# Kernel tuning notes

Hardware: AMD Instinct MI355X
Metric: run time of the kernel (lower is better)

Reference implementation:

```python
import jax, jax.numpy as jnp
import numpy as np
from jax import lax

B_, L_, D_ = 4, 2048, 256
DI, NS, DC, DTR = 512, 16, 4, 16  # d_inner=2*D, d_state, d_conv, dt_rank=ceil(D/16)
DFF = 4 * D_


def setup_inputs():
    key = jax.random.key(0)
    ks = jax.random.split(key, 20)
    rn = lambda k, s, sc=0.02: jax.random.normal(k, s, jnp.float32) * sc
    return {
        "x": jax.random.normal(ks[0], (B_, L_, D_), jnp.float32),
        "in_proj_w": rn(ks[1], (2 * DI, D_)), "in_proj_b": jnp.zeros((2 * DI,), jnp.float32),
        "conv_w": rn(ks[2], (DI, DC), 0.1), "conv_b": jnp.zeros((DI,), jnp.float32),
        "x_proj_w": rn(ks[3], (DTR + 2 * NS, DI)),
        "dt_proj_w": rn(ks[4], (DI, DTR), 0.1), "dt_proj_b": rn(ks[5], (DI,), 0.5),
        "A_log": jnp.log(jnp.tile(jnp.arange(1, NS + 1, dtype=jnp.float32), (DI, 1))),
        "D_ssm": jnp.ones((DI,), jnp.float32),
        "out_proj_w": rn(ks[6], (D_, DI)), "out_proj_b": jnp.zeros((D_,), jnp.float32),
        "ln1_g": jnp.ones((D_,), jnp.float32), "ln1_b": jnp.zeros((D_,), jnp.float32),
        "fc1_w": rn(ks[7], (DFF, D_)), "fc1_b": jnp.zeros((DFF,), jnp.float32),
        "fc2_w": rn(ks[8], (D_, DFF)), "fc2_b": jnp.zeros((D_,), jnp.float32),
        "ln2_g": jnp.ones((D_,), jnp.float32), "ln2_b": jnp.zeros((D_,), jnp.float32),
    }


def _layer_norm(x, g, b, eps=1e-5):
    m = jnp.mean(x, -1, keepdims=True)
    v = jnp.mean((x - m) ** 2, -1, keepdims=True)
    return (x - m) / jnp.sqrt(v + eps) * g + b


def _mamba(x, in_proj_w, in_proj_b, conv_w, conv_b, x_proj_w, dt_proj_w, dt_proj_b, A_log, D_ssm, out_proj_w, out_proj_b):
    B, L, D = x.shape
    xz = x @ in_proj_w.T + in_proj_b                       # [B,L,2*DI]
    xi, z = jnp.split(xz, 2, axis=-1)
    # causal depthwise conv over time
    xc = jnp.transpose(xi, (0, 2, 1))                       # [B,DI,L]
    xc = lax.conv_general_dilated(xc, conv_w[:, None, :], (1,), [(DC - 1, 0)],
                                  dimension_numbers=("NCH", "OIH", "NCH"),
                                  feature_group_count=DI)
    xi = jax.nn.silu(jnp.transpose(xc + conv_b[None, :, None], (0, 2, 1)))  # [B,L,DI]
    x_dbl = xi @ x_proj_w.T                                 # [B,L,DTR+2*NS]
    dt, Bs, Cs = jnp.split(x_dbl, [DTR, DTR + NS], axis=-1)
    dt = jax.nn.softplus(dt @ dt_proj_w.T + dt_proj_b)      # [B,L,DI]
    A = -jnp.exp(A_log)                                     # [DI,NS]
    dA = jnp.exp(dt[..., None] * A)                         # [B,L,DI,NS]
    dBu = dt[..., None] * Bs[:, :, None, :] * xi[..., None]  # [B,L,DI,NS]
    dA_t = jnp.moveaxis(dA, 1, 0)
    dBu_t = jnp.moveaxis(dBu, 1, 0)
    C_t = jnp.moveaxis(Cs, 1, 0)                            # [L,B,NS]

    def step(h, inp):
        a, bu, c = inp
        h = a * h + bu                                      # [B,DI,NS]
        y = jnp.einsum("bdn,bn->bd", h, c)
        return h, y

    h0 = jnp.zeros((B, DI, NS), x.dtype)
    _, ys = lax.scan(step, h0, (dA_t, dBu_t, C_t))
    y = jnp.moveaxis(ys, 0, 1) + xi * D_ssm                 # [B,L,DI]
    y = y * jax.nn.silu(z)
    return y @ out_proj_w.T + out_proj_b


def reference(x, in_proj_w, in_proj_b, conv_w, conv_b, x_proj_w, dt_proj_w, dt_proj_b,
              A_log, D_ssm, out_proj_w, out_proj_b, ln1_g, ln1_b, fc1_w, fc1_b,
              fc2_w, fc2_b, ln2_g, ln2_b):
    gelu = lambda t: jax.nn.gelu(t, approximate=False)
    ssm = _mamba(x, in_proj_w, in_proj_b, conv_w, conv_b, x_proj_w, dt_proj_w,
                 dt_proj_b, A_log, D_ssm, out_proj_w, out_proj_b)
    y = _layer_norm(x + ssm, ln1_g, ln1_b)                  # dropout = identity (eval)
    ffn = gelu(gelu(y @ fc1_w.T + fc1_b) @ fc2_w.T + fc2_b)
    return _layer_norm(y + ffn, ln2_g, ln2_b)
```

## Files before the change

### kernel.cpp

```cpp
#include <hip/hip_runtime.h>

typedef __bf16 bf16x8 __attribute__((ext_vector_type(8)));
typedef float  f32x4  __attribute__((ext_vector_type(4)));

#define AS1 __attribute__((address_space(1)))
#define AS3 __attribute__((address_space(3)))

__device__ __forceinline__ float bf2f(ushort u) {
    union { unsigned int i; float f; } v; v.i = ((unsigned int)u) << 16; return v.f;
}
__device__ __forceinline__ ushort f2bf(float f) {
    union { float f; unsigned int i; } v; v.f = f;
    unsigned int i = v.i;
    unsigned int r = i + 0x7FFFu + ((i >> 16) & 1u);
    return (ushort)(r >> 16);
}
__device__ __forceinline__ float bflo(unsigned int u) { return bf2f((ushort)(u & 0xFFFFu)); }
__device__ __forceinline__ float bfhi(unsigned int u) { return bf2f((ushort)(u >> 16)); }
__device__ __forceinline__ float gelu_f(float v) {
    return 0.5f * v * (1.f + erff(v * 0.70710678118654752f));
}

__device__ __forceinline__ bool sniff_inline(const ushort* __restrict__ x) {
    const int lane = threadIdx.x & 63;
    int cnt = 0;
    #pragma unroll
    for (int r = 0; r < 4; r++) {
        const ushort u = x[lane + r * 64];
        const int e = (u >> 7) & 0xFF;
        if ((u & 0x7FFF) == 0 || (e >= 112 && e <= 141)) cnt++;
    }
    #pragma unroll
    for (int o = 32; o > 0; o >>= 1) cnt += __shfl_xor(cnt, o);
    return cnt >= 224;
}

struct CanonArgs {
    const void* src[20];
    int off[20];
    int total;
};

__launch_bounds__(256)
__global__ void canon_k(CanonArgs a, ushort* __restrict__ dst, ushort* __restrict__ xpw_pad,
                        const ushort* __restrict__ sniffx)
{
    const int i = blockIdx.x * 256 + threadIdx.x;
    if (i >= a.total) {
        const int j = i - a.total;
        if (j < 8192) xpw_pad[24576 + j] = 0;
        return;
    }
    const bool fl = sniff_inline(sniffx);
    int s = 0;
    #pragma unroll
    for (int t = 1; t < 20; t++) if (i >= a.off[t]) s = t;
    const int li = i - a.off[s];
    ushort v;
    if (fl) v = ((const ushort*)a.src[s])[li];
    else    v = f2bf(((const float*)a.src[s])[li]);
    dst[i] = v;
    if (s == 5) xpw_pad[li] = v;
}

template<int BM, int BN>
__launch_bounds__(256, 2)
__global__ void gemm_bt(const ushort* __restrict__ A, const ushort* __restrict__ W,
                        const ushort* __restrict__ bias, ushort* __restrict__ Cb,
                        int N, int K)
{
    constexpr int WMT = BM / 32;
    constexpr int WNT = BN / 32;
    __shared__ __align__(16) ushort As[BM * 32];
    __shared__ __align__(16) ushort Bs[BN * 32];
    const int tid  = threadIdx.x;
    const int wave = tid >> 6;
    const int lane = tid & 63;
    const int m0 = blockIdx.x * BM;
    const int n0 = blockIdx.y * BN;
    const int wm = (wave >> 1) * (BM / 2);
    const int wn = (wave & 1) * (BN / 2);
    const int lrow = lane & 15;
    const int quad = lane >> 4;

    f32x4 acc[WMT][WNT];
    #pragma unroll
    for (int i = 0; i < WMT; i++)
        #pragma unroll
        for (int j = 0; j < WNT; j++)
            #pragma unroll
            for (int r = 0; r < 4; r++) acc[i][j][r] = 0.f;

    for (int k0 = 0; k0 < K; k0 += 32) {
        #pragma unroll
        for (int t = 0; t < BM / 64; t++) {
            const int inst = t * 4 + wave;
            const int row  = inst * 16 + (lane >> 2);
            const int sub  = lane & 3;
            const ushort* gp = A + (size_t)(m0 + row) * K + (k0 + sub * 8);
            __builtin_amdgcn_global_load_lds((AS1 void*)(void*)gp,
                                             (AS3 void*)(As + inst * 512), 16, 0, 0);
        }
        #pragma unroll
        for (int t = 0; t < BN / 64; t++) {
            const int inst = t * 4 + wave;
            const int row  = inst * 16 + (lane >> 2);
            const int sub  = lane & 3;
            const ushort* gp = W + (size_t)(n0 + row) * K + (k0 + sub * 8);
            __builtin_amdgcn_global_load_lds((AS1 void*)(void*)gp,
                                             (AS3 void*)(Bs + inst * 512), 16, 0, 0);
        }
        __syncthreads();
        bf16x8 afr[WMT], bfr[WNT];
        #pragma unroll
        for (int i = 0; i < WMT; i++)
            afr[i] = *(const bf16x8*)&As[(wm + i * 16 + lrow) * 32 + quad * 8];
        #pragma unroll
        for (int j = 0; j < WNT; j++)
            bfr[j] = *(const bf16x8*)&Bs[(wn + j * 16 + lrow) * 32 + quad * 8];
        #pragma unroll
        for (int i = 0; i < WMT; i++)
            #pragma unroll
            for (int j = 0; j < WNT; j++)
                acc[i][j] = __builtin_amdgcn_mfma_f32_16x16x32_bf16(afr[i], bfr[j], acc[i][j], 0, 0, 0);
        __syncthreads();
    }

    #pragma unroll
    for (int i = 0; i < WMT; i++) {
        const int gm = m0 + wm + i * 16 + quad * 4;
        #pragma unroll
        for (int j = 0; j < WNT; j++) {
            const int gn = n0 + wn + j * 16 + lrow;
            const float bv = bf2f(bias[gn]);
            #pragma unroll
            for (int r = 0; r < 4; r++)
                Cb[(size_t)(gm + r) * N + gn] = f2bf(acc[i][j][r] + bv);
        }
    }
}

__launch_bounds__(512)
__global__ void convscan1_k(const ushort* __restrict__ xz, const ushort* __restrict__ cw,
                            const ushort* __restrict__ cb, const ushort* __restrict__ xpw_pad,
                            const ushort* __restrict__ dtw, const ushort* __restrict__ dtb,
                            const ushort* __restrict__ Alog,
                            float* __restrict__ xdbl, float* __restrict__ summ)
{
    __shared__ __align__(16) ushort xcs[32 * 520];
    __shared__ float XD[32 * 48];
    const int tid  = threadIdx.x;
    const int wave = tid >> 6;
    const int lane = tid & 63;
    const int lrow = lane & 15;
    const int quad = lane >> 4;
    const int c = blockIdx.x, b = blockIdx.y;
    const int t0 = b * 2048 + c * 32;

    {
        const int d8 = (tid & 63) * 8;
        ushort wl[32];
        *(uint4*)&wl[0]  = *(const uint4*)&cw[d8 * 4];
        *(uint4*)&wl[8]  = *(const uint4*)&cw[d8 * 4 + 8];
        *(uint4*)&wl[16] = *(const uint4*)&cw[d8 * 4 + 16];
        *(uint4*)&wl[24] = *(const uint4*)&cw[d8 * 4 + 24];
        ushort bl[8];
        *(uint4*)&bl[0] = *(const uint4*)&cb[d8];
        #pragma unroll
        for (int it = 0; it < 4; it++) {
            const int trow = it * 8 + (tid >> 6);
            const int t = t0 + trow;
            const int l = t & 2047;
            float acc[8];
            #pragma unroll
            for (int j = 0; j < 8; j++) acc[j] = bf2f(bl[j]);
            #pragma unroll
            for (int k = 0; k < 4; k++) {
                const int ls = l - 3 + k;
                if (ls >= 0) {
                    ushort xl[8];
                    *(uint4*)&xl[0] = *(const uint4*)&xz[(size_t)(t - 3 + k) * 1024 + d8];
                    #pragma unroll
                    for (int j = 0; j < 8; j++) acc[j] += bf2f(xl[j]) * bf2f(wl[j * 4 + k]);
                }
            }
            ushort ol[8];
            #pragma unroll
            for (int j = 0; j < 8; j++) {
                const float s = acc[j] / (1.f + __expf(-acc[j]));
                ol[j] = f2bf(s);
            }
            *(uint4*)&xcs[trow * 520 + d8] = *(uint4*)&ol[0];
        }
    }
    __syncthreads();

    {
        const int mt = wave >> 2, nt = wave & 3;
        const ushort* bptr = xpw_pad + (size_t)(nt * 16 + lrow) * 512 + quad * 8;
        f32x4 acc = {0.f, 0.f, 0.f, 0.f};
        bf16x8 bn = *(const bf16x8*)bptr;
        for (int k0 = 0; k0 < 512; k0 += 32) {
            const bf16x8 bc = bn;
            if (k0 + 32 < 512) bn = *(const bf16x8*)(bptr + k0 + 32);
            const bf16x8 afr = *(const bf16x8*)&xcs[(mt * 16 + lrow) * 520 + k0 + quad * 8];
            acc = __builtin_amdgcn_mfma_f32_16x16x32_bf16(afr, bc, acc, 0, 0, 0);
        }
        const int col = nt * 16 + lrow;
        if (col < 48) {
            #pragma unroll
            for (int r = 0; r < 4; r++) {
                const int row = mt * 16 + quad * 4 + r;
                XD[row * 48 + col] = acc[r];
                xdbl[(size_t)(t0 + row) * 64 + col] = acc[r];
            }
        }
    }
    __syncthreads();

    {
        const int d = tid;
        const uint4 w0 = *(const uint4*)&dtw[d * 16];
        const uint4 w1 = *(const uint4*)&dtw[d * 16 + 8];
        const float wd[16] = { bflo(w0.x), bfhi(w0.x), bflo(w0.y), bfhi(w0.y),
                               bflo(w0.z), bfhi(w0.z), bflo(w0.w), bfhi(w0.w),
                               bflo(w1.x), bfhi(w1.x), bflo(w1.y), bfhi(w1.y),
                               bflo(w1.z), bfhi(w1.z), bflo(w1.w), bfhi(w1.w) };
        const float dtbv = bf2f(dtb[d]);
        float A[16], h[16];
        #pragma unroll
        for (int n = 0; n < 16; n++) {
            A[n] = -__expf(bf2f(Alog[d * 16 + n]));
            h[n] = 0.f;
        }
        float sdt = 0.f;
        for (int i = 0; i < 32; i++) {
            const float* Xr = &XD[i * 48];
            float s = dtbv;
            #pragma unroll
            for (int k = 0; k < 16; k++) s += Xr[k] * wd[k];
            const float dtv = (s > 15.f) ? s : __logf(1.f + __expf(s));
            const float xiv = bf2f(xcs[i * 520 + d]);
            const float dx = dtv * xiv;
            sdt += dtv;
            #pragma unroll
            for (int n = 0; n < 16; n++) {
                const float da = __expf(dtv * A[n]);
                h[n] = da * h[n] + dx * Xr[16 + n];
            }
        }
        const size_t base = ((size_t)(b * 64 + c) * 32) * 512 + d;
        #pragma unroll
        for (int n = 0; n < 16; n++) summ[base + (size_t)n * 512] = __expf(A[n] * sdt);
        #pragma unroll
        for (int n = 0; n < 16; n++) summ[base + (size_t)(16 + n) * 512] = h[n];
    }
}

__launch_bounds__(512)
__global__ void combine_k(float* __restrict__ summ)
{
    const int b = blockIdx.x >> 4, n = blockIdx.x & 15;
    const int d = threadIdx.x;
    float h = 0.f;
    #pragma unroll
    for (int half = 0; half < 2; half++) {
        float p[32], hl[32], ho[32];
        #pragma unroll
        for (int c2 = 0; c2 < 32; c2++) {
            const size_t sb = ((size_t)((b * 64 + half * 32 + c2) * 32 + n)) * 512 + d;
            p[c2]  = summ[sb];
            hl[c2] = summ[sb + 8192];
        }
        #pragma unroll
        for (int c2 = 0; c2 < 32; c2++) {
            ho[c2] = h;
            h = p[c2] * h + hl[c2];
        }
        #pragma unroll
        for (int c2 = 0; c2 < 32; c2++) {
            const size_t sb = ((size_t)((b * 64 + half * 32 + c2) * 32 + n)) * 512 + d;
            summ[sb] = ho[c2];
        }
    }
}

__launch_bounds__(512)
__global__ void tail_k(const ushort* __restrict__ xz, const ushort* __restrict__ cw,
                       const ushort* __restrict__ cb, const float* __restrict__ xdbl,
                       const ushort* __restrict__ dtw, const ushort* __restrict__ dtb,
                       const ushort* __restrict__ Alog, const float* __restrict__ summ,
                       const ushort* __restrict__ Dssm, const ushort* __restrict__ cx,
                       const ushort* __restrict__ opw, const ushort* __restrict__ opb,
                       const ushort* __restrict__ ln1g, const ushort* __restrict__ ln1b,
                       const ushort* __restrict__ f1w, const ushort* __restrict__ f1b,
                       const ushort* __restrict__ f2w, const ushort* __restrict__ f2b,
                       const ushort* __restrict__ ln2g, const ushort* __restrict__ ln2b,
                       void* __restrict__ dout, const ushort* __restrict__ sniffx)
{
    __shared__ __align__(16) ushort yls[32 * 520];
    __shared__ float XD[32 * 48];
    __shared__ __align__(16) ushort y1bs[32 * 264];
    __shared__ float redS[8 * 32], redQ[8 * 32];
    ushort* f1q = yls;

    const int tid  = threadIdx.x;
    const int wave = tid >> 6;
    const int lane = tid & 63;
    const int lrow = lane & 15;
    const int quad = lane >> 4;
    const int c = blockIdx.x, b = blockIdx.y;
    const int t0 = b * 2048 + c * 32;
    const int n0w = wave * 32;

    {
        const int d8 = (tid & 63) * 8;
        ushort wl[32];
        *(uint4*)&wl[0]  = *(const uint4*)&cw[d8 * 4];
        *(uint4*)&wl[8]  = *(const uint4*)&cw[d8 * 4 + 8];
        *(uint4*)&wl[16] = *(const uint4*)&cw[d8 * 4 + 16];
        *(uint4*)&wl[24] = *(const uint4*)&cw[d8 * 4 + 24];
        ushort bl[8];
        *(uint4*)&bl[0] = *(const uint4*)&cb[d8];
        #pragma unroll
        for (int it = 0; it < 4; it++) {
            const int trow = it * 8 + (tid >> 6);
            const int t = t0 + trow;
            const int l = t & 2047;
            float acc[8];
            #pragma unroll
            for (int j = 0; j < 8; j++) acc[j] = bf2f(bl[j]);
            #pragma unroll
            for (int k = 0; k < 4; k++) {
                const int ls = l - 3 + k;
                if (ls >= 0) {
                    ushort xl[8];
                    *(uint4*)&xl[0] = *(const uint4*)&xz[(size_t)(t - 3 + k) * 1024 + d8];
                    #pragma unroll
                    for (int j = 0; j < 8; j++) acc[j] += bf2f(xl[j]) * bf2f(wl[j * 4 + k]);
                }
            }
            ushort ol[8];
            #pragma unroll
            for (int j = 0; j < 8; j++) {
                const float s = acc[j] / (1.f + __expf(-acc[j]));
                ol[j] = f2bf(s);
            }
            *(uint4*)&yls[trow * 520 + d8] = *(uint4*)&ol[0];
        }
    }
    for (int e = tid; e < 1536; e += 512)
        XD[e] = xdbl[(size_t)(t0 + (e / 48)) * 64 + (e % 48)];
    __syncthreads();

    {
        const int d = tid;
        const uint4 w0 = *(const uint4*)&dtw[d * 16];
        const uint4 w1 = *(const uint4*)&dtw[d * 16 + 8];
        const float wd[16] = { bflo(w0.x), bfhi(w0.x), bflo(w0.y), bfhi(w0.y),
                               bflo(w0.z), bfhi(w0.z), bflo(w0.w), bfhi(w0.w),
                               bflo(w1.x), bfhi(w1.x), bflo(w1.y), bfhi(w1.y),
                               bflo(w1.z), bfhi(w1.z), bflo(w1.w), bfhi(w1.w) };
        const float dtbv = bf2f(dtb[d]);
        float A[16], h[16];
        #pragma unroll
        for (int n = 0; n < 16; n++) A[n] = -__expf(bf2f(Alog[d * 16 + n]));
        const size_t base = ((size_t)(b * 64 + c) * 32) * 512 + d;
        #pragma unroll
        for (int n = 0; n < 16; n++) h[n] = summ[base + (size_t)n * 512];
        const float Dv = bf2f(Dssm[d]);
        for (int i = 0; i < 32; i++) {
            const int t = t0 + i;
            const float* Xr = &XD[i * 48];
            float s = dtbv;
            #pragma unroll
            for (int k = 0; k < 16; k++) s += Xr[k] * wd[k];
            const float dtv = (s > 15.f) ? s : __logf(1.f + __expf(s));
            const float xiv = bf2f(yls[i * 520 + d]);
            const float dx = dtv * xiv;
            float yv = 0.f;
            #pragma unroll
            for (int n = 0; n < 16; n++) {
                const float da = __expf(dtv * A[n]);
                h[n] = da * h[n] + dx * Xr[16 + n];
                yv += h[n] * Xr[32 + n];
            }
            yv += xiv * Dv;
            const float zv = bf2f(xz[(size_t)t * 1024 + 512 + d]);
            yv *= zv / (1.f + __expf(-zv));
            yls[i * 520 + d] = f2bf(yv);
        }
    }
    __syncthreads();

    f32x4 accP[2][2];
    #pragma unroll
    for (int i = 0; i < 2; i++)
        #pragma unroll
        for (int j = 0; j < 2; j++)
            #pragma unroll
            for (int r = 0; r < 4; r++) accP[i][j][r] = 0.f;
    {
        const ushort* bp0 = opw + (size_t)(n0w + lrow) * 512 + quad * 8;
        const ushort* bp1 = opw + (size_t)(n0w + 16 + lrow) * 512 + quad * 8;
        bf16x8 bn0 = *(const bf16x8*)bp0;
        bf16x8 bn1 = *(const bf16x8*)bp1;
        for (int k0 = 0; k0 < 512; k0 += 32) {
            const bf16x8 bc0 = bn0, bc1 = bn1;
            if (k0 + 32 < 512) {
                bn0 = *(const bf16x8*)(bp0 + k0 + 32);
                bn1 = *(const bf16x8*)(bp1 + k0 + 32);
            }
            bf16x8 afr[2];
            #pragma unroll
            for (int i = 0; i < 2; i++)
                afr[i] = *(const bf16x8*)&yls[(i * 16 + lrow) * 520 + k0 + quad * 8];
            #pragma unroll
            for (int i = 0; i < 2; i++) {
                accP[i][0] = __builtin_amdgcn_mfma_f32_16x16x32_bf16(afr[i], bc0, accP[i][0], 0, 0, 0);
                accP[i][1] = __builtin_amdgcn_mfma_f32_16x16x32_bf16(afr[i], bc1, accP[i][1], 0, 0, 0);
            }
        }
    }
    float vP[2][2][4];
    float ps[2][4], pq[2][4];
    #pragma unroll
    for (int i = 0; i < 2; i++)
        #pragma unroll
        for (int r = 0; r < 4; r++) { ps[i][r] = 0.f; pq[i][r] = 0.f; }
    #pragma unroll
    for (int i = 0; i < 2; i++) {
        #pragma unroll
        for (int j = 0; j < 2; j++) {
            const int col = n0w + j * 16 + lrow;
            const float bv = bf2f(opb[col]);
            #pragma unroll
            for (int r = 0; r < 4; r++) {
                const int row = i * 16 + quad * 4 + r;
                float v = accP[i][j][r] + bv + bf2f(cx[(size_t)(t0 + row) * 256 + col]);
                vP[i][j][r] = v;
                ps[i][r] += v;
                pq[i][r] += v * v;
            }
        }
    }
    #pragma unroll
    for (int i = 0; i < 2; i++)
        #pragma unroll
        for (int r = 0; r < 4; r++) {
            #pragma unroll
            for (int o = 8; o > 0; o >>= 1) {
                ps[i][r] += __shfl_xor(ps[i][r], o);
                pq[i][r] += __shfl_xor(pq[i][r], o);
            }
            if (lrow == 0) {
                const int row = i * 16 + quad * 4 + r;
                redS[wave * 32 + row] = ps[i][r];
                redQ[wave * 32 + row] = pq[i][r];
            }
        }
    __syncthreads();

    float y1f[2][2][4];
    #pragma unroll
    for (int i = 0; i < 2; i++) {
        #pragma unroll
        for (int r = 0; r < 4; r++) {
            const int row = i * 16 + quad * 4 + r;
            float S = 0.f, Q = 0.f;
            #pragma unroll
            for (int w = 0; w < 8; w++) { S += redS[w * 32 + row]; Q += redQ[w * 32 + row]; }
            const float mean = S * (1.f / 256.f);
            const float var  = Q * (1.f / 256.f) - mean * mean;
            const float rs   = rsqrtf(var + 1e-5f);
            #pragma unroll
            for (int j = 0; j < 2; j++) {
                const int col = n0w + j * 16 + lrow;
                const float o2 = (vP[i][j][r] - mean) * rs * bf2f(ln1g[col]) + bf2f(ln1b[col]);
                y1f[i][j][r] = o2;
                y1bs[row * 264 + col] = f2bf(o2);
            }
        }
    }
    __syncthreads();

    f32x4 acc2[2][2];
    #pragma unroll
    for (int i = 0; i < 2; i++)
        #pragma unroll
        for (int j = 0; j < 2; j++)
            #pragma unroll
            for (int r = 0; r < 4; r++) acc2[i][j][r] = 0.f;

    for (int q = 0; q < 4; q++) {
        f32x4 a1[2][2];
        #pragma unroll
        for (int i = 0; i < 2; i++)
            #pragma unroll
            for (int j = 0; j < 2; j++)
                #pragma unroll
                for (int r = 0; r < 4; r++) a1[i][j][r] = 0.f;
        {
            const ushort* bp0 = f1w + (size_t)(q * 256 + n0w + lrow) * 256 + quad * 8;
            const ushort* bp1 = f1w + (size_t)(q * 256 + n0w + 16 + lrow) * 256 + quad * 8;
            bf16x8 bn0 = *(const bf16x8*)bp0;
            bf16x8 bn1 = *(const bf16x8*)bp1;
            for (int k0 = 0; k0 < 256; k0 += 32) {
                const bf16x8 bc0 = bn0, bc1 = bn1;
                if (k0 + 32 < 256) {
                    bn0 = *(const bf16x8*)(bp0 + k0 + 32);
                    bn1 = *(const bf16x8*)(bp1 + k0 + 32);
                }
                bf16x8 afr[2];
                #pragma unroll
                for (int i = 0; i < 2; i++)
                    afr[i] = *(const bf16x8*)&y1bs[(i * 16 + lrow) * 264 + k0 + quad * 8];
                #pragma unroll
                for (int i = 0; i < 2; i++) {
                    a1[i][0] = __builtin_amdgcn_mfma_f32_16x16x32_bf16(afr[i], bc0, a1[i][0], 0, 0, 0);
                    a1[i][1] = __builtin_amdgcn_mfma_f32_16x16x32_bf16(afr[i], bc1, a1[i][1], 0, 0, 0);
                }
            }
        }
        #pragma unroll
        for (int i = 0; i < 2; i++)
            #pragma unroll
            for (int j = 0; j < 2; j++) {
                const int qc = n0w + j * 16 + lrow;
                const float bv = bf2f(f1b[q * 256 + qc]);
                #pragma unroll
                for (int r = 0; r < 4; r++) {
                    const int row = i * 16 + quad * 4 + r;
                    f1q[row * 260 + qc] = f2bf(gelu_f(a1[i][j][r] + bv));
                }
            }
        __syncthreads();
        {
            const ushort* bp0 = f2w + (size_t)(n0w + lrow) * 1024 + q * 256 + quad * 8;
            const ushort* bp1 = f2w + (size_t)(n0w + 16 + lrow) * 1024 + q * 256 + quad * 8;
            bf16x8 bn0 = *(const bf16x8*)bp0;
            bf16x8 bn1 = *(const bf16x8*)bp1;
            for (int k0 = 0; k0 < 256; k0 += 32) {
                const bf16x8 bc0 = bn0, bc1 = bn1;
                if (k0 + 32 < 256) {
                    bn0 = *(const bf16x8*)(bp0 + k0 + 32);
                    bn1 = *(const bf16x8*)(bp1 + k0 + 32);
                }
                bf16x8 afr[2];
                #pragma unroll
                for (int i = 0; i < 2; i++)
                    afr[i] = *(const bf16x8*)&f1q[(i * 16 + lrow) * 260 + k0 + quad * 8];
                #pragma unroll
                for (int i = 0; i < 2; i++) {
                    acc2[i][0] = __builtin_amdgcn_mfma_f32_16x16x32_bf16(afr[i], bc0, acc2[i][0], 0, 0, 0);
                    acc2[i][1] = __builtin_amdgcn_mfma_f32_16x16x32_bf16(afr[i], bc1, acc2[i][1], 0, 0, 0);
                }
            }
        }
        __syncthreads();
    }

    float v2[2][2][4];
    #pragma unroll
    for (int i = 0; i < 2; i++)
        #pragma unroll
        for (int r = 0; r < 4; r++) { ps[i][r] = 0.f; pq[i][r] = 0.f; }
    #pragma unroll
    for (int i = 0; i < 2; i++)
        #pragma unroll
        for (int j = 0; j < 2; j++) {
            const int col = n0w + j * 16 + lrow;
            const float bv = bf2f(f2b[col]);
            #pragma unroll
            for (int r = 0; r < 4; r++) {
                const float v = gelu_f(acc2[i][j][r] + bv) + y1f[i][j][r];
                v2[i][j][r] = v;
                ps[i][r] += v;
                pq[i][r] += v * v;
            }
        }
    #pragma unroll
    for (int i = 0; i < 2; i++)
        #pragma unroll
        for (int r = 0; r < 4; r++) {
            #pragma unroll
            for (int o = 8; o > 0; o >>= 1) {
                ps[i][r] += __shfl_xor(ps[i][r], o);
                pq[i][r] += __shfl_xor(pq[i][r], o);
            }
            if (lrow == 0) {
                const int row = i * 16 + quad * 4 + r;
                redS[wave * 32 + row] = ps[i][r];
                redQ[wave * 32 + row] = pq[i][r];
            }
        }
    __syncthreads();

    const bool fl = sniff_inline(sniffx);
    #pragma unroll
    for (int i = 0; i < 2; i++) {
        #pragma unroll
        for (int r = 0; r < 4; r++) {
            const int row = i * 16 + quad * 4 + r;
            float S = 0.f, Q = 0.f;
            #pragma unroll
            for (int w = 0; w < 8; w++) { S += redS[w * 32 + row]; Q += redQ[w * 32 + row]; }
            const float mean = S * (1.f / 256.f);
            const float var  = Q * (1.f / 256.f) - mean * mean;
            const float rs   = rsqrtf(var + 1e-5f);
            #pragma unroll
            for (int j = 0; j < 2; j++) {
                const int col = n0w + j * 16 + lrow;
                const size_t off = (size_t)(t0 + row) * 256 + col;
                const float o2 = (v2[i][j][r] - mean) * rs * bf2f(ln2g[col]) + bf2f(ln2b[col]);
                if (fl) ((ushort*)dout)[off] = f2bf(o2);
                else    ((float*)dout)[off]  = o2;
            }
        }
    }
}

extern "C" void kernel_launch(void* const* d_in, const int* in_sizes, int n_in,
                              void* d_out, int out_size, void* d_ws, size_t ws_size,
                              hipStream_t stream)
{
    char* ws = (char*)d_ws;
    ushort* canon = (ushort*)(ws + 256);

    static const int coff[20] = {
        0,        2097152,  2359296,  2360320,  2362368,
        2362880,  2387456,  2395648,  2396160,  2404352,
        2404864,  2535936,  2536192,  2536448,  2536704,
        2798848,  2799872,  3062016,  3062272,  3062528 };
    static const int ctot = 3062784;

    CanonArgs ca;
    for (int i = 0; i < 20; i++) { ca.src[i] = d_in[i]; ca.off[i] = coff[i]; }
    ca.total = ctot;

    const ushort* cx   = canon + coff[0];
    const ushort* cipw = canon + coff[1];
    const ushort* cipb = canon + coff[2];
    const ushort* ccw  = canon + coff[3];
    const ushort* ccb  = canon + coff[4];
    const ushort* cdtw = canon + coff[6];
    const ushort* cdtb = canon + coff[7];
    const ushort* calog= canon + coff[8];
    const ushort* cdssm= canon + coff[9];
    const ushort* copw = canon + coff[10];
    const ushort* copb = canon + coff[11];
    const ushort* cln1g= canon + coff[12];
    const ushort* cln1b= canon + coff[13];
    const ushort* cf1w = canon + coff[14];
    const ushort* cf1b = canon + coff[15];
    const ushort* cf2w = canon + coff[16];
    const ushort* cf2b = canon + coff[17];
    const ushort* cln2g= canon + coff[18];
    const ushort* cln2b= canon + coff[19];

    ushort* xpw_pad = (ushort*)(ws + 6291456);
    ushort* xz      = (ushort*)(ws + 8388608);
    float*  xdbl    = (float*)(ws + 25165824);
    float*  summ    = (float*)(ws + 27262976);
    const ushort* sx = (const ushort*)d_in[0];

    canon_k<<<(ctot + 8192 + 255) / 256, 256, 0, stream>>>(ca, canon, xpw_pad, sx);
    gemm_bt<128, 128><<<dim3(64, 8), 256, 0, stream>>>(cx, cipw, cipb, xz, 1024, 256);
    convscan1_k<<<dim3(64, 4), 512, 0, stream>>>(
        xz, ccw, ccb, xpw_pad, cdtw, cdtb, calog, xdbl, summ);
    combine_k<<<64, 512, 0, stream>>>(summ);
    tail_k<<<dim3(64, 4), 512, 0, stream>>>(
        xz, ccw, ccb, xdbl, cdtw, cdtb, calog, summ, cdssm, cx,
        copw, copb, cln1g, cln1b, cf1w, cf1b, cf2w, cf2b, cln2g, cln2b,
        d_out, sx);
}
```

Before: 238.8 us.

## Halve scan chunk length to 16 tokens, doubling grid blocks

Chunk size for the chunked selective scan and the fused tail kernel drops from 32 to 16 timesteps, so both kernels launch 512 blocks instead of 256 and fill more of the GPU. The chunk summary now stores only the per-chunk dt sum instead of 16 decay products, and the combine kernel recomputes the decays with exp. The cost is a longer serial carry in combine (128 chunks per sequence), more redundant weight loads across blocks, and half the MFMA work per wave in the tail GEMMs, so weight reuse drops.

Result: slower. 258.8 us (+8.4%).

```diff
diff --git a/kernel.cpp b/kernel.cpp
--- a/kernel.cpp
+++ b/kernel.cpp
@@ -145,17 +145,18 @@
                             const ushort* __restrict__ cb, const ushort* __restrict__ xpw_pad,
                             const ushort* __restrict__ dtw, const ushort* __restrict__ dtb,
                             const ushort* __restrict__ Alog,
-                            float* __restrict__ xdbl, float* __restrict__ summ)
+                            float* __restrict__ xdbl, float* __restrict__ summh,
+                            float* __restrict__ sdtb)
 {
-    __shared__ __align__(16) ushort xcs[32 * 520];
-    __shared__ float XD[32 * 48];
+    __shared__ __align__(16) ushort xcs[16 * 520];
+    __shared__ float XD[16 * 48];
     const int tid  = threadIdx.x;
     const int wave = tid >> 6;
     const int lane = tid & 63;
     const int lrow = lane & 15;
     const int quad = lane >> 4;
     const int c = blockIdx.x, b = blockIdx.y;
-    const int t0 = b * 2048 + c * 32;
+    const int t0 = b * 2048 + c * 16;
 
     {
         const int d8 = (tid & 63) * 8;
@@ -167,8 +168,8 @@
         ushort bl[8];
         *(uint4*)&bl[0] = *(const uint4*)&cb[d8];
         #pragma unroll
-        for (int it = 0; it < 4; it++) {
-            const int trow = it * 8 + (tid >> 6);
+        for (int it = 0; it < 2; it++) {
+            const int trow = it * 8 + wave;
             const int t = t0 + trow;
             const int l = t & 2047;
             float acc[8];
@@ -195,25 +196,23 @@
     }
     __syncthreads();
 
-    {
-        const int mt = wave >> 2, nt = wave & 3;
+    if (wave < 3) {
+        const int nt = wave;
         const ushort* bptr = xpw_pad + (size_t)(nt * 16 + lrow) * 512 + quad * 8;
         f32x4 acc = {0.f, 0.f, 0.f, 0.f};
         bf16x8 bn = *(const bf16x8*)bptr;
         for (int k0 = 0; k0 < 512; k0 += 32) {
             const bf16x8 bc = bn;
             if (k0 + 32 < 512) bn = *(const bf16x8*)(bptr + k0 + 32);
-            const bf16x8 afr = *(const bf16x8*)&xcs[(mt * 16 + lrow) * 520 + k0 + quad * 8];
+            const bf16x8 afr = *(const bf16x8*)&xcs[lrow * 520 + k0 + quad * 8];
             acc = __builtin_amdgcn_mfma_f32_16x16x32_bf16(afr, bc, acc, 0, 0, 0);
         }
         const int col = nt * 16 + lrow;
-        if (col < 48) {
-            #pragma unroll
-            for (int r = 0; r < 4; r++) {
-                const int row = mt * 16 + quad * 4 + r;
-                XD[row * 48 + col] = acc[r];
-                xdbl[(size_t)(t0 + row) * 64 + col] = acc[r];
-            }
+        #pragma unroll
+        for (int r = 0; r < 4; r++) {
+            const int row = quad * 4 + r;
+            XD[row * 48 + col] = acc[r];
+            xdbl[(size_t)(t0 + row) * 64 + col] = acc[r];
         }
     }
     __syncthreads();
@@ -234,7 +233,7 @@
             h[n] = 0.f;
         }
         float sdt = 0.f;
-        for (int i = 0; i < 32; i++) {
+        for (int i = 0; i < 16; i++) {
             const float* Xr = &XD[i * 48];
             float s = dtbv;
             #pragma unroll
@@ -249,28 +248,29 @@
                 h[n] = da * h[n] + dx * Xr[16 + n];
             }
         }
-        const size_t base = ((size_t)(b * 64 + c) * 32) * 512 + d;
-        #pragma unroll
-        for (int n = 0; n < 16; n++) summ[base + (size_t)n * 512] = __expf(A[n] * sdt);
-        #pragma unroll
-        for (int n = 0; n < 16; n++) summ[base + (size_t)(16 + n) * 512] = h[n];
+        const size_t bh = ((size_t)(b * 128 + c) * 16) * 512 + d;
+        #pragma unroll
+        for (int n = 0; n < 16; n++) summh[bh + (size_t)n * 512] = h[n];
+        sdtb[(size_t)(b * 128 + c) * 512 + d] = sdt;
     }
 }
 
 __launch_bounds__(512)
-__global__ void combine_k(float* __restrict__ summ)
+__global__ void combine_k(float* __restrict__ summh, const float* __restrict__ sdtb,
+                          const ushort* __restrict__ Alog)
 {
     const int b = blockIdx.x >> 4, n = blockIdx.x & 15;
     const int d = threadIdx.x;
+    const float An = -__expf(bf2f(Alog[d * 16 + n]));
     float h = 0.f;
     #pragma unroll
-    for (int half = 0; half < 2; half++) {
+    for (int q = 0; q < 4; q++) {
         float p[32], hl[32], ho[32];
         #pragma unroll
         for (int c2 = 0; c2 < 32; c2++) {
-            const size_t sb = ((size_t)((b * 64 + half * 32 + c2) * 32 + n)) * 512 + d;
-            p[c2]  = summ[sb];
-            hl[c2] = summ[sb + 8192];
+            const int cc = q * 32 + c2;
+            hl[c2] = summh[((size_t)(b * 128 + cc) * 16 + n) * 512 + d];
+            p[c2]  = __expf(An * sdtb[(size_t)(b * 128 + cc) * 512 + d]);
         }
         #pragma unroll
         for (int c2 = 0; c2 < 32; c2++) {
@@ -278,10 +278,8 @@
             h = p[c2] * h + hl[c2];
         }
         #pragma unroll
-        for (int c2 = 0; c2 < 32; c2++) {
-            const size_t sb = ((size_t)((b * 64 + half * 32 + c2) * 32 + n)) * 512 + d;
-            summ[sb] = ho[c2];
-        }
+        for (int c2 = 0; c2 < 32; c2++)
+            summh[((size_t)(b * 128 + (q * 32 + c2)) * 16 + n) * 512 + d] = ho[c2];
     }
 }
 
@@ -289,7 +287,7 @@
 __global__ void tail_k(const ushort* __restrict__ xz, const ushort* __restrict__ cw,
                        const ushort* __restrict__ cb, const float* __restrict__ xdbl,
                        const ushort* __restrict__ dtw, const ushort* __restrict__ dtb,
-                       const ushort* __restrict__ Alog, const float* __restrict__ summ,
+                       const ushort* __restrict__ Alog, const float* __restrict__ summh,
                        const ushort* __restrict__ Dssm, const ushort* __restrict__ cx,
                        const ushort* __restrict__ opw, const ushort* __restrict__ opb,
                        const ushort* __restrict__ ln1g, const ushort* __restrict__ ln1b,
@@ -298,10 +296,10 @@
                        const ushort* __restrict__ ln2g, const ushort* __restrict__ ln2b,
                        void* __restrict__ dout, const ushort* __restrict__ sniffx)
 {
-    __shared__ __align__(16) ushort yls[32 * 520];
-    __shared__ float XD[32 * 48];
-    __shared__ __align__(16) ushort y1bs[32 * 264];
-    __shared__ float redS[8 * 32], redQ[8 * 32];
+    __shared__ __align__(16) ushort yls[16 * 520];
+    __shared__ float XD[16 * 48];
+    __shared__ __align__(16) ushort y1bs[16 * 264];
+    __shared__ float redS[8 * 16], redQ[8 * 16];
     ushort* f1q = yls;
 
     const int tid  = threadIdx.x;
@@ -310,7 +308,7 @@
     const int lrow = lane & 15;
     const int quad = lane >> 4;
     const int c = blockIdx.x, b = blockIdx.y;
-    const int t0 = b * 2048 + c * 32;
+    const int t0 = b * 2048 + c * 16;
     const int n0w = wave * 32;
 
     {
@@ -323,8 +321,8 @@
         ushort bl[8];
         *(uint4*)&bl[0] = *(const uint4*)&cb[d8];
         #pragma unroll
-        for (int it = 0; it < 4; it++) {
-            const int trow = it * 8 + (tid >> 6);
+        for (int it = 0; it < 2; it++) {
+            const int trow = it * 8 + wave;
             const int t = t0 + trow;
             const int l = t & 2047;
             float acc[8];
@@ -349,7 +347,7 @@
             *(uint4*)&yls[trow * 520 + d8] = *(uint4*)&ol[0];
         }
     }
-    for (int e = tid; e < 1536; e += 512)
+    for (int e = tid; e < 768; e += 512)
         XD[e] = xdbl[(size_t)(t0 + (e / 48)) * 64 + (e % 48)];
     __syncthreads();
 
@@ -365,11 +363,11 @@
         float A[16], h[16];
         #pragma unroll
         for (int n = 0; n < 16; n++) A[n] = -__expf(bf2f(Alog[d * 16 + n]));
-        const size_t base = ((size_t)(b * 64 + c) * 32) * 512 + d;
-        #pragma unroll
-        for (int n = 0; n < 16; n++) h[n] = summ[base + (size_t)n * 512];
+        const size_t bh = ((size_t)(b * 128 + c) * 16) * 512 + d;
+        #pragma unroll
+        for (int n = 0; n < 16; n++) h[n] = summh[bh + (size_t)n * 512];
         const float Dv = bf2f(Dssm[d]);
-        for (int i = 0; i < 32; i++) {
+        for (int i = 0; i < 16; i++) {
             const int t = t0 + i;
             const float* Xr = &XD[i * 48];
             float s = dtbv;
@@ -393,13 +391,11 @@
     }
     __syncthreads();
 
-    f32x4 accP[2][2];
-    #pragma unroll
-    for (int i = 0; i < 2; i++)
-        #pragma unroll
-        for (int j = 0; j < 2; j++)
-            #pragma unroll
-            for (int r = 0; r < 4; r++) accP[i][j][r] = 0.f;
+    f32x4 accP[2];
+    #pragma unroll
+    for (int j = 0; j < 2; j++)
+        #pragma unroll
+        for (int r = 0; r < 4; r++) accP[j][r] = 0.f;
     {
         const ushort* bp0 = opw + (size_t)(n0w + lrow) * 512 + quad * 8;
         const ushort* bp1 = opw + (size_t)(n0w + 16 + lrow) * 512 + quad * 8;
@@ -411,95 +407,75 @@
                 bn0 = *(const bf16x8*)(bp0 + k0 + 32);
                 bn1 = *(const bf16x8*)(bp1 + k0 + 32);
             }
-            bf16x8 afr[2];
-            #pragma unroll
-            for (int i = 0; i < 2; i++)
-                afr[i] = *(const bf16x8*)&yls[(i * 16 + lrow) * 520 + k0 + quad * 8];
-            #pragma unroll
-            for (int i = 0; i < 2; i++) {
-                accP[i][0] = __builtin_amdgcn_mfma_f32_16x16x32_bf16(afr[i], bc0, accP[i][0], 0, 0, 0);
-                accP[i][1] = __builtin_amdgcn_mfma_f32_16x16x32_bf16(afr[i], bc1, accP[i][1], 0, 0, 0);
-            }
-        }
-    }
-    float vP[2][2][4];
-    float ps[2][4], pq[2][4];
-    #pragma unroll
-    for (int i = 0; i < 2; i++)
-        #pragma unroll
-        for (int r = 0; r < 4; r++) { ps[i][r] = 0.f; pq[i][r] = 0.f; }
-    #pragma unroll
-    for (int i = 0; i < 2; i++) {
+            const bf16x8 afr = *(const bf16x8*)&yls[lrow * 520 + k0 + quad * 8];
+            accP[0] = __builtin_amdgcn_mfma_f32_16x16x32_bf16(afr, bc0, accP[0], 0, 0, 0);
+            accP[1] = __builtin_amdgcn_mfma_f32_16x16x32_bf16(afr, bc1, accP[1], 0, 0, 0);
+        }
+    }
+    float vP[2][4];
+    float ps[4], pq[4];
+    #pragma unroll
+    for (int r = 0; r < 4; r++) { ps[r] = 0.f; pq[r] = 0.f; }
+    #pragma unroll
+    for (int j = 0; j < 2; j++) {
+        const int col = n0w + j * 16 + lrow;
+        const float bv = bf2f(opb[col]);
+        #pragma unroll
+        for (int r = 0; r < 4; r++) {
+            const int row = quad * 4 + r;
+            float v = accP[j][r] + bv + bf2f(cx[(size_t)(t0 + row) * 256 + col]);
+            vP[j][r] = v;
+            ps[r] += v;
+            pq[r] += v * v;
+        }
+    }
+    #pragma unroll
+    for (int r = 0; r < 4; r++) {
+        #pragma unroll
+        for (int o = 8; o > 0; o >>= 1) {
+            ps[r] += __shfl_xor(ps[r], o);
+            pq[r] += __shfl_xor(pq[r], o);
+        }
+        if (lrow == 0) {
+            const int row = quad * 4 + r;
+            redS[wave * 16 + row] = ps[r];
+            redQ[wave * 16 + row] = pq[r];
+        }
+    }
+    __syncthreads();
+
+    float y1f[2][4];
+    #pragma unroll
+    for (int r = 0; r < 4; r++) {
+        const int row = quad * 4 + r;
+        float S = 0.f, Q = 0.f;
+        #pragma unroll
+        for (int w = 0; w < 8; w++) { S += redS[w * 16 + row]; Q += redQ[w * 16 + row]; }
+        const float mean = S * (1.f / 256.f);
+        const float var  = Q * (1.f / 256.f) - mean * mean;
+        const float rs   = rsqrtf(var + 1e-5f);
         #pragma unroll
         for (int j = 0; j < 2; j++) {
             const int col = n0w + j * 16 + lrow;
-            const float bv = bf2f(opb[col]);
-            #pragma unroll
-            for (int r = 0; r < 4; r++) {
-                const int row = i * 16 + quad * 4 + r;
-                float v = accP[i][j][r] + bv + bf2f(cx[(size_t)(t0 + row) * 256 + col]);
-                vP[i][j][r] = v;
-                ps[i][r] += v;
-                pq[i][r] += v * v;
-            }
-        }
-    }
-    #pragma unroll
-    for (int i = 0; i < 2; i++)
-        #pragma unroll
-        for (int r = 0; r < 4; r++) {
-            #pragma unroll
-            for (int o = 8; o > 0; o >>= 1) {
-                ps[i][r] += __shfl_xor(ps[i][r], o);
-                pq[i][r] += __shfl_xor(pq[i][r], o);
-            }
-            if (lrow == 0) {
-                const int row = i * 16 + quad * 4 + r;
-                redS[wave * 32 + row] = ps[i][r];
-                redQ[wave * 32 + row] = pq[i][r];
-            }
-        }
+            const float o2 = (vP[j][r] - mean) * rs * bf2f(ln1g[col]) + bf2f(ln1b[col]);
+            y1f[j][r] = o2;
+            y1bs[row * 264 + col] = f2bf(o2);
+        }
+    }
     __syncthreads();
 
-    float y1f[2][2][4];
-    #pragma unroll
-    for (int i = 0; i < 2; i++) {
-        #pragma unroll
-        for (int r = 0; r < 4; r++) {
-            const int row = i * 16 + quad * 4 + r;
-            float S = 0.f, Q = 0.f;
-            #pragma unroll
-            for (int w = 0; w < 8; w++) { S += redS[w * 32 + row]; Q += redQ[w * 32 + row]; }
-            const float mean = S * (1.f / 256.f);
-            const float var  = Q * (1.f / 256.f) - mean * mean;
-            const float rs   = rsqrtf(var + 1e-5f);
-            #pragma unroll
-            for (int j = 0; j < 2; j++) {
-                const int col = n0w + j * 16 + lrow;
-                const float o2 = (vP[i][j][r] - mean) * rs * bf2f(ln1g[col]) + bf2f(ln1b[col]);
-                y1f[i][j][r] = o2;
-                y1bs[row * 264 + col] = f2bf(o2);
-            }
-        }
-    }
-    __syncthreads();
-
-    f32x4 acc2[2][2];
-    #pragma unroll
-    for (int i = 0; i < 2; i++)
+    f32x4 acc2[2];
+    #pragma unroll
+    for (int j = 0; j < 2; j++)
+        #pragma unroll
+        for (int r = 0; r < 4; r++) acc2[j][r] = 0.f;
+
+    for (int q = 0; q < 4; q++) {
+        f32x4 a1[2];
         #pragma unroll
         for (int j = 0; j < 2; j++)
             #pragma unroll
-            for (int r = 0; r < 4; r++) acc2[i][j][r] = 0.f;
-
-    for (int q = 0; q < 4; q++) {
-        f32x4 a1[2][2];
-        #pragma unroll
-        for (int i = 0; i < 2; i++)
-            #pragma unroll
-            for (int j = 0; j < 2; j++)
-                #pragma unroll
-                for (int r = 0; r < 4; r++) a1[i][j][r] = 0.f;
+            for (int r = 0; r < 4; r++) a1[j][r] = 0.f;
         {
             const ushort* bp0 = f1w + (size_t)(q * 256 + n0w + lrow) * 256 + quad * 8;
             const ushort* bp1 = f1w + (size_t)(q * 256 + n0w + 16 + lrow) * 256 + quad * 8;
@@ -511,29 +487,21 @@
                     bn0 = *(const bf16x8*)(bp0 + k0 + 32);
                     bn1 = *(const bf16x8*)(bp1 + k0 + 32);
                 }
-                bf16x8 afr[2];
-                #pragma unroll
-                for (int i = 0; i < 2; i++)
-                    afr[i] = *(const bf16x8*)&y1bs[(i * 16 + lrow) * 264 + k0 + quad * 8];
-                #pragma unroll
-                for (int i = 0; i < 2; i++) {
-                    a1[i][0] = __builtin_amdgcn_mfma_f32_16x16x32_bf16(afr[i], bc0, a1[i][0], 0, 0, 0);
-                    a1[i][1] = __builtin_amdgcn_mfma_f32_16x16x32_bf16(afr[i], bc1, a1[i][1], 0, 0, 0);
-                }
-            }
-        }
-        #pragma unroll
-        for (int i = 0; i < 2; i++)
-            #pragma unroll
-            for (int j = 0; j < 2; j++) {
-                const int qc = n0w + j * 16 + lrow;
-                const float bv = bf2f(f1b[q * 256 + qc]);
-                #pragma unroll
-                for (int r = 0; r < 4; r++) {
-                    const int row = i * 16 + quad * 4 + r;
-                    f1q[row * 260 + qc] = f2bf(gelu_f(a1[i][j][r] + bv));
-                }
-            }
+                const bf16x8 afr = *(const bf16x8*)&y1bs[lrow * 264 + k0 + quad * 8];
+                a1[0] = __builtin_amdgcn_mfma_f32_16x16x32_bf16(afr, bc0, a1[0], 0, 0, 0);
+                a1[1] = __builtin_amdgcn_mfma_f32_16x16x32_bf16(afr, bc1, a1[1], 0, 0, 0);
+            }
+        }
+        #pragma unroll
+        for (int j = 0; j < 2; j++) {
+            const int qc = n0w + j * 16 + lrow;
+            const float bv = bf2f(f1b[q * 256 + qc]);
+            #pragma unroll
+            for (int r = 0; r < 4; r++) {
+                const int row = quad * 4 + r;
+                f1q[row * 260 + qc] = f2bf(gelu_f(a1[j][r] + bv));
+            }
+        }
         __syncthreads();
         {
             const ushort* bp0 = f2w + (size_t)(n0w + lrow) * 1024 + q * 256 + quad * 8;
@@ -546,76 +514,61 @@
                     bn0 = *(const bf16x8*)(bp0 + k0 + 32);
                     bn1 = *(const bf16x8*)(bp1 + k0 + 32);
                 }
-                bf16x8 afr[2];
-                #pragma unroll
-                for (int i = 0; i < 2; i++)
-                    afr[i] = *(const bf16x8*)&f1q[(i * 16 + lrow) * 260 + k0 + quad * 8];
-                #pragma unroll
-                for (int i = 0; i < 2; i++) {
-                    acc2[i][0] = __builtin_amdgcn_mfma_f32_16x16x32_bf16(afr[i], bc0, acc2[i][0], 0, 0, 0);
-                    acc2[i][1] = __builtin_amdgcn_mfma_f32_16x16x32_bf16(afr[i], bc1, acc2[i][1], 0, 0, 0);
-                }
+                const bf16x8 afr = *(const bf16x8*)&f1q[lrow * 260 + k0 + quad * 8];
+                acc2[0] = __builtin_amdgcn_mfma_f32_16x16x32_bf16(afr, bc0, acc2[0], 0, 0, 0);
+                acc2[1] = __builtin_amdgcn_mfma_f32_16x16x32_bf16(afr, bc1, acc2[1], 0, 0, 0);
             }
         }
         __syncthreads();
     }
 
-    float v2[2][2][4];
-    #pragma unroll
-    for (int i = 0; i < 2; i++)
-        #pragma unroll
-        for (int r = 0; r < 4; r++) { ps[i][r] = 0.f; pq[i][r] = 0.f; }
-    #pragma unroll
-    for (int i = 0; i < 2; i++)
+    float v2[2][4];
+    #pragma unroll
+    for (int r = 0; r < 4; r++) { ps[r] = 0.f; pq[r] = 0.f; }
+    #pragma unroll
+    for (int j = 0; j < 2; j++) {
+        const int col = n0w + j * 16 + lrow;
+        const float bv = bf2f(f2b[col]);
+        #pragma unroll
+        for (int r = 0; r < 4; r++) {
+            const float v = gelu_f(acc2[j][r] + bv) + y1f[j][r];
+            v2[j][r] = v;
+            ps[r] += v;
+            pq[r] += v * v;
+        }
+    }
+    #pragma unroll
+    for (int r = 0; r < 4; r++) {
+        #pragma unroll
+        for (int o = 8; o > 0; o >>= 1) {
+            ps[r] += __shfl_xor(ps[r], o);
+            pq[r] += __shfl_xor(pq[r], o);
+        }
+        if (lrow == 0) {
+            const int row = quad * 4 + r;
+            redS[wave * 16 + row] = ps[r];
+            redQ[wave * 16 + row] = pq[r];
+        }
+    }
+    __syncthreads();
+
+    const bool fl = sniff_inline(sniffx);
+    #pragma unroll
+    for (int r = 0; r < 4; r++) {
+        const int row = quad * 4 + r;
+        float S = 0.f, Q = 0.f;
+        #pragma unroll
+        for (int w = 0; w < 8; w++) { S += redS[w * 16 + row]; Q += redQ[w * 16 + row]; }
+        const float mean = S * (1.f / 256.f);
+        const float var  = Q * (1.f / 256.f) - mean * mean;
+        const float rs   = rsqrtf(var + 1e-5f);
         #pragma unroll
         for (int j = 0; j < 2; j++) {
             const int col = n0w + j * 16 + lrow;
-            const float bv = bf2f(f2b[col]);
-            #pragma unroll
-            for (int r = 0; r < 4; r++) {
-                const float v = gelu_f(acc2[i][j][r] + bv) + y1f[i][j][r];
-                v2[i][j][r] = v;
-                ps[i][r] += v;
-                pq[i][r] += v * v;
-            }
-        }
-    #pragma unroll
-    for (int i = 0; i < 2; i++)
-        #pragma unroll
-        for (int r = 0; r < 4; r++) {
-            #pragma unroll
-            for (int o = 8; o > 0; o >>= 1) {
-                ps[i][r] += __shfl_xor(ps[i][r], o);
-                pq[i][r] += __shfl_xor(pq[i][r], o);
-            }
-            if (lrow == 0) {
-                const int row = i * 16 + quad * 4 + r;
-                redS[wave * 32 + row] = ps[i][r];
-                redQ[wave * 32 + row] = pq[i][r];
-            }
-        }
-    __syncthreads();
-
-    const bool fl = sniff_inline(sniffx);
-    #pragma unroll
-    for (int i = 0; i < 2; i++) {
-        #pragma unroll
-        for (int r = 0; r < 4; r++) {
-            const int row = i * 16 + quad * 4 + r;
-            float S = 0.f, Q = 0.f;
-            #pragma unroll
-            for (int w = 0; w < 8; w++) { S += redS[w * 32 + row]; Q += redQ[w * 32 + row]; }
-            const float mean = S * (1.f / 256.f);
-            const float var  = Q * (1.f / 256.f) - mean * mean;
-            const float rs   = rsqrtf(var + 1e-5f);
-            #pragma unroll
-            for (int j = 0; j < 2; j++) {
-                const int col = n0w + j * 16 + lrow;
-                const size_t off = (size_t)(t0 + row) * 256 + col;
-                const float o2 = (v2[i][j][r] - mean) * rs * bf2f(ln2g[col]) + bf2f(ln2b[col]);
-                if (fl) ((ushort*)dout)[off] = f2bf(o2);
-                else    ((float*)dout)[off]  = o2;
-            }
+            const size_t off = (size_t)(t0 + row) * 256 + col;
+            const float o2 = (v2[j][r] - mean) * rs * bf2f(ln2g[col]) + bf2f(ln2b[col]);
+            if (fl) ((ushort*)dout)[off] = f2bf(o2);
+            else    ((float*)dout)[off]  = o2;
         }
     }
 }
@@ -661,16 +614,17 @@
     ushort* xpw_pad = (ushort*)(ws + 6291456);
     ushort* xz      = (ushort*)(ws + 8388608);
     float*  xdbl    = (float*)(ws + 25165824);
-    float*  summ    = (float*)(ws + 27262976);
+    float*  summh   = (float*)(ws + 27262976);
+    float*  sdtb    = (float*)(ws + 44040192);
     const ushort* sx = (const ushort*)d_in[0];
 
     canon_k<<<(ctot + 8192 + 255) / 256, 256, 0, stream>>>(ca, canon, xpw_pad, sx);
     gemm_bt<128, 128><<<dim3(64, 8), 256, 0, stream>>>(cx, cipw, cipb, xz, 1024, 256);
-    convscan1_k<<<dim3(64, 4), 512, 0, stream>>>(
-        xz, ccw, ccb, xpw_pad, cdtw, cdtb, calog, xdbl, summ);
-    combine_k<<<64, 512, 0, stream>>>(summ);
-    tail_k<<<dim3(64, 4), 512, 0, stream>>>(
-        xz, ccw, ccb, xdbl, cdtw, cdtb, calog, summ, cdssm, cx,
+    convscan1_k<<<dim3(128, 4), 512, 0, stream>>>(
+        xz, ccw, ccb, xpw_pad, cdtw, cdtb, calog, xdbl, summh, sdtb);
+    combine_k<<<64, 512, 0, stream>>>(summh, sdtb, calog);
+    tail_k<<<dim3(128, 4), 512, 0, stream>>>(
+        xz, ccw, ccb, xdbl, cdtw, cdtb, calog, summh, cdssm, cx,
         copw, copb, cln1g, cln1b, cf1w, cf1b, cf2w, cf2b, cln2g, cln2b,
         d_out, sx);
 }
```
